# Optimization experiments

Measured on AMD Instinct MI355X. Metric: run time of the kernel, lower is better.

## Reference

```python
import jax, jax.numpy as jnp
import numpy as np
import math

CHUNK = 64

def _linear(x, W, b):
    # torch nn.Linear: y = x @ W.T + b
    return jnp.einsum('bsd,ed->bse', x, W) + b

def setup_inputs() -> dict:
    key = jax.random.key(0)
    ks = jax.random.split(key, 10)
    B, S, D = 4, 4096, 512
    scale = 0.02
    inp = {
        'x': jax.random.normal(ks[0], (B, S, D), jnp.float32),
        'base_phases': jax.random.normal(ks[1], (S, D), jnp.float32) * math.pi,
        'Wk': jax.random.normal(ks[2], (D, D), jnp.float32) * scale,
        'bk': jnp.zeros((D,), jnp.float32),
        'Wv': jax.random.normal(ks[3], (D, D), jnp.float32) * scale,
        'bv': jnp.zeros((D,), jnp.float32),
        'Wq': jax.random.normal(ks[4], (D, D), jnp.float32) * scale,
        'bq': jnp.zeros((D,), jnp.float32),
        'Wkm': jax.random.normal(ks[5], (D, D), jnp.float32) * scale,
        'bkm': jnp.zeros((D,), jnp.float32),
        'Wqm': jax.random.normal(ks[6], (D, D), jnp.float32) * scale,
        'bqm': jnp.zeros((D,), jnp.float32),
        'mod_scale': jnp.ones((1,), jnp.float32) * 0.1,
        'ln_g': jnp.ones((D,), jnp.float32),
        'ln_b': jnp.zeros((D,), jnp.float32),
        'Wo': jax.random.normal(ks[7], (D, D), jnp.float32) * scale,
        'bo': jnp.zeros((D,), jnp.float32),
    }
    return inp

def reference(x, base_phases, Wk, bk, Wv, bv, Wq, bq, Wkm, bkm, Wqm, bqm, mod_scale, ln_g, ln_b, Wo, bo):
    B, S, D = x.shape
    bp = base_phases[:S][None]                      # [1,S,D]
    key = _linear(x, Wk, bk)
    value = _linear(x, Wv, bv)
    query = _linear(x, Wq, bq)
    key_phase = bp + _linear(key, Wkm, bkm) * mod_scale
    query_phase = bp + _linear(query, Wqm, bqm) * mod_scale
    bound_real = value * jnp.cos(key_phase)
    bound_imag = value * jnp.sin(key_phase)
    # chunked cumulative memory (S divisible by CHUNK -> no padding)
    nC = S // CHUNK
    br = bound_real.reshape(B, nC, CHUNK, D)
    bi = bound_imag.reshape(B, nC, CHUNK, D)
    qp = query_phase.reshape(B, nC, CHUNK, D)
    mem_real = jnp.cumsum(br, axis=2)
    mem_imag = jnp.cumsum(bi, axis=2)
    retrieved = (mem_real * jnp.cos(qp) + mem_imag * jnp.sin(qp)).reshape(B, S, D)
    retrieved = retrieved / math.sqrt(D)
    # LayerNorm + Linear (to_out)
    mu = jnp.mean(retrieved, axis=-1, keepdims=True)
    var = jnp.mean((retrieved - mu) ** 2, axis=-1, keepdims=True)
    normed = (retrieved - mu) / jnp.sqrt(var + 1e-5) * ln_g + ln_b
    out = _linear(normed, Wo, bo)
    return x + out
```

## Files before the change

kernel.cpp:

```cpp
#include <hip/hip_runtime.h>
#include <hip/hip_bf16.h>


typedef __attribute__((ext_vector_type(8))) short short8;
typedef __attribute__((ext_vector_type(4))) float f32x4;

#define M_TOK   16384
#define DIM     512
#define NCHUNK  64
#define RPAD    520

__device__ __forceinline__ void gll16(const void* g, void* l) {
  __builtin_amdgcn_global_load_lds(
      (const __attribute__((address_space(1))) unsigned int*)g,
      (__attribute__((address_space(3))) unsigned int*)l, 16, 0, 0);
}

__device__ __forceinline__ uint2 pack4bf(float4 v) {
  union { __hip_bfloat16 h[4]; uint2 u; } t;
  t.h[0] = __float2bfloat16(v.x);
  t.h[1] = __float2bfloat16(v.y);
  t.h[2] = __float2bfloat16(v.z);
  t.h[3] = __float2bfloat16(v.w);
  return t.u;
}

__global__ __launch_bounds__(256) void prep_all(
    const float* __restrict__ x, __hip_bfloat16* __restrict__ x_bf,
    const float* __restrict__ Wv, const float* __restrict__ Wo,
    const float* __restrict__ bv,
    const float* __restrict__ Wkm, const float* __restrict__ Wqm,
    const float* __restrict__ Wk, const float* __restrict__ Wq,
    const float* __restrict__ bk, const float* __restrict__ bkm,
    const float* __restrict__ bq, const float* __restrict__ bqm,
    __hip_bfloat16* __restrict__ Wall, float* __restrict__ bc1,
    __hip_bfloat16* __restrict__ Wm_bf, __hip_bfloat16* __restrict__ WT_bf) {
  const int tid = threadIdx.x;
  if (blockIdx.x < 8192) {
    int i = blockIdx.x * 256 + tid;
    ((uint2*)x_bf)[i] = pack4bf(((const float4*)x)[i]);
    return;
  }
  const int b = blockIdx.x - 8192;
  if (b < 512) {
    int m = b >> 8;
    int idx = ((b & 255) * 256 + tid) * 4;
    const float* src = m ? Wo : Wv;
    __hip_bfloat16* dst = Wall + (m ? (size_t)1536 * 512 : 0);
    ((uint2*)dst)[idx >> 2] = pack4bf(*(const float4*)(src + idx));
    int t = b * 256 + tid;
    if (t < 512) bc1[t] = bv[t];
  } else if (b < 1024) {
    int bb = b - 512;
    int m = bb >> 8;
    int idx = ((bb & 255) * 256 + tid) * 4;
    const float* src = m ? Wqm : Wkm;
    ((uint2*)(Wm_bf + (size_t)m * 262144))[idx >> 2] =
        pack4bf(*(const float4*)(src + idx));
  } else if (b < 1152) {
    __shared__ float tile[64][65];
    int bb = b - 1024;
    int z = bb >> 6;
    int tl = bb & 63;
    int tr = tl >> 3, tc = tl & 7;
    const float* src = z ? Wq : Wk;
#pragma unroll
    for (int i = 0; i < 4; i++) {
      int r = (tid >> 4) + 16 * i;
      int c4 = (tid & 15) * 4;
      float4 v = *(const float4*)(src + (size_t)(tr * 64 + r) * 512 +
                                  tc * 64 + c4);
      tile[r][c4 + 0] = v.x;
      tile[r][c4 + 1] = v.y;
      tile[r][c4 + 2] = v.z;
      tile[r][c4 + 3] = v.w;
    }
    __syncthreads();
    int orow = tid >> 2;
    int seg = tid & 3;
    __hip_bfloat16* dst = WT_bf + (size_t)z * 262144 +
                          (size_t)(tc * 64 + orow) * 512 + tr * 64 + seg * 16;
#pragma unroll
    for (int q = 0; q < 4; q++) {
      float4 v;
      v.x = tile[seg * 16 + q * 4 + 0][orow];
      v.y = tile[seg * 16 + q * 4 + 1][orow];
      v.z = tile[seg * 16 + q * 4 + 2][orow];
      v.w = tile[seg * 16 + q * 4 + 3][orow];
      *(uint2*)(dst + q * 4) = pack4bf(v);
    }
  } else {
    int row = (b - 1152) * 4 + (tid >> 6);
    int lane = tid & 63;
    int z = row >> 9;
    int i = row & 511;
    const float* Wm = z ? Wqm : Wkm;
    const float* b0 = z ? bq : bk;
    const float* bm = z ? bqm : bkm;
    const float4* w4 = (const float4*)(Wm + (size_t)i * 512 + lane * 8);
    const float4* v4 = (const float4*)(b0 + lane * 8);
    float4 w0 = w4[0], w1 = w4[1], c0 = v4[0], c1 = v4[1];
    float acc = w0.x * c0.x + w0.y * c0.y + w0.z * c0.z + w0.w * c0.w +
                w1.x * c1.x + w1.y * c1.y + w1.z * c1.z + w1.w * c1.w;
#pragma unroll
    for (int off = 32; off; off >>= 1) acc += __shfl_xor(acc, off, 64);
    if (lane == 0) bc1[512 + z * 512 + i] = acc + bm[i];
  }
}

__global__ __launch_bounds__(256) void gemm_bt(
    const __hip_bfloat16* __restrict__ A, int lda,
    const __hip_bfloat16* __restrict__ Bt,
    const float* __restrict__ bias,
    __hip_bfloat16* __restrict__ Cout, int ldc) {
  constexpr int K = 512, BK = 32;
  __shared__ __align__(16) __hip_bfloat16 As[128 * BK];
  __shared__ __align__(16) __hip_bfloat16 Bs[128 * BK];

  const int tid  = threadIdx.x;
  const int lane = tid & 63;
  const int w    = tid >> 6;
  const int wm   = w >> 1;
  const int wn   = w & 1;
  const int m0   = blockIdx.y * 128;
  const int n0   = blockIdx.x * 128;

  const int rS0    = (w * 2 + 0) * 16 + (lane >> 2);
  const int rS1    = (w * 2 + 1) * 16 + (lane >> 2);
  const int kInRow = (lane & 3) * 8;
  const __hip_bfloat16* gA0 = A + (size_t)(m0 + rS0) * lda + kInRow;
  const __hip_bfloat16* gA1 = A + (size_t)(m0 + rS1) * lda + kInRow;
  const __hip_bfloat16* gB0 = Bt + (size_t)(n0 + rS0) * K + kInRow;
  const __hip_bfloat16* gB1 = Bt + (size_t)(n0 + rS1) * K + kInRow;
  char* ldsA0 = (char*)As + (w * 2 + 0) * 1024;
  char* ldsA1 = (char*)As + (w * 2 + 1) * 1024;
  char* ldsB0 = (char*)Bs + (w * 2 + 0) * 1024;
  char* ldsB1 = (char*)Bs + (w * 2 + 1) * 1024;

  f32x4 acc[4][4] = {};

  const int rfA = lane & 15;
  const int rfK = (lane >> 4) * 8;

  for (int kt = 0; kt < K; kt += BK) {
    __syncthreads();
    gll16(gA0 + kt, ldsA0);
    gll16(gA1 + kt, ldsA1);
    gll16(gB0 + kt, ldsB0);
    gll16(gB1 + kt, ldsB1);
    __syncthreads();

    short8 af[4], bf[4];
#pragma unroll
    for (int i = 0; i < 4; i++)
      af[i] = *(const short8*)(As + (wm * 64 + i * 16 + rfA) * BK + rfK);
#pragma unroll
    for (int j = 0; j < 4; j++)
      bf[j] = *(const short8*)(Bs + (wn * 64 + j * 16 + rfA) * BK + rfK);
#pragma unroll
    for (int i = 0; i < 4; i++)
#pragma unroll
      for (int j = 0; j < 4; j++)
        acc[i][j] = __builtin_amdgcn_mfma_f32_16x16x32_bf16(
            af[i], bf[j], acc[i][j], 0, 0, 0);
  }

  const int cq = lane >> 4;
#pragma unroll
  for (int i = 0; i < 4; i++) {
    int row = m0 + wm * 64 + i * 16 + cq * 4;
#pragma unroll
    for (int j = 0; j < 4; j++) {
      int col = n0 + wn * 64 + j * 16 + (lane & 15);
      float bz = bias[col];
#pragma unroll
      for (int r = 0; r < 4; r++) {
        float v = acc[i][j][r] + bz;
        Cout[(size_t)(row + r) * ldc + col] = __float2bfloat16(v);
      }
    }
  }
}

__global__ __launch_bounds__(256) void gemm_compose(
    const __hip_bfloat16* __restrict__ Wm_bf,
    const __hip_bfloat16* __restrict__ WT_bf,
    __hip_bfloat16* __restrict__ Wall) {
  constexpr int K = 512, BK = 32;
  const __hip_bfloat16* A  = Wm_bf + (size_t)blockIdx.z * 262144;
  const __hip_bfloat16* Bt = WT_bf + (size_t)blockIdx.z * 262144;
  __hip_bfloat16* C = Wall + (size_t)(512 + blockIdx.z * 512) * 512;
  __shared__ __align__(16) __hip_bfloat16 As[128 * BK];
  __shared__ __align__(16) __hip_bfloat16 Bs[128 * BK];

  const int tid  = threadIdx.x;
  const int lane = tid & 63;
  const int w    = tid >> 6;
  const int wm   = w >> 1;
  const int wn   = w & 1;
  const int m0   = blockIdx.y * 128;
  const int n0   = blockIdx.x * 128;

  const int rS0    = (w * 2 + 0) * 16 + (lane >> 2);
  const int rS1    = (w * 2 + 1) * 16 + (lane >> 2);
  const int kInRow = (lane & 3) * 8;
  const __hip_bfloat16* gA0 = A + (size_t)(m0 + rS0) * K + kInRow;
  const __hip_bfloat16* gA1 = A + (size_t)(m0 + rS1) * K + kInRow;
  const __hip_bfloat16* gB0 = Bt + (size_t)(n0 + rS0) * K + kInRow;
  const __hip_bfloat16* gB1 = Bt + (size_t)(n0 + rS1) * K + kInRow;
  char* ldsA0 = (char*)As + (w * 2 + 0) * 1024;
  char* ldsA1 = (char*)As + (w * 2 + 1) * 1024;
  char* ldsB0 = (char*)Bs + (w * 2 + 0) * 1024;
  char* ldsB1 = (char*)Bs + (w * 2 + 1) * 1024;

  f32x4 acc[4][4] = {};
  const int rfA = lane & 15;
  const int rfK = (lane >> 4) * 8;

  for (int kt = 0; kt < K; kt += BK) {
    __syncthreads();
    gll16(gA0 + kt, ldsA0);
    gll16(gA1 + kt, ldsA1);
    gll16(gB0 + kt, ldsB0);
    gll16(gB1 + kt, ldsB1);
    __syncthreads();

    short8 af[4], bf[4];
#pragma unroll
    for (int i = 0; i < 4; i++)
      af[i] = *(const short8*)(As + (wm * 64 + i * 16 + rfA) * BK + rfK);
#pragma unroll
    for (int j = 0; j < 4; j++)
      bf[j] = *(const short8*)(Bs + (wn * 64 + j * 16 + rfA) * BK + rfK);
#pragma unroll
    for (int i = 0; i < 4; i++)
#pragma unroll
      for (int j = 0; j < 4; j++)
        acc[i][j] = __builtin_amdgcn_mfma_f32_16x16x32_bf16(
            af[i], bf[j], acc[i][j], 0, 0, 0);
  }

  const int cq = lane >> 4;
#pragma unroll
  for (int i = 0; i < 4; i++) {
    int row = m0 + wm * 64 + i * 16 + cq * 4;
#pragma unroll
    for (int j = 0; j < 4; j++) {
      int col = n0 + wn * 64 + j * 16 + (lane & 15);
#pragma unroll
      for (int r = 0; r < 4; r++)
        C[(size_t)(row + r) * 512 + col] = __float2bfloat16(acc[i][j][r]);
    }
  }
}

__global__ __launch_bounds__(1024) void fused_pg(
    const __hip_bfloat16* __restrict__ VKQ,
    const float* __restrict__ bp,
    const float* __restrict__ mod_scale,
    const float* __restrict__ ln_g, const float* __restrict__ ln_b,
    const __hip_bfloat16* __restrict__ WoB,
    const float* __restrict__ bo,
    const float* __restrict__ x,
    float* __restrict__ out) {
  __shared__ __hip_bfloat16 R[64 * RPAD];
  __shared__ float Tr[512], Ti[512];
  const int tid    = threadIdx.x;
  const int seg    = tid >> 9;
  const int d      = tid & 511;
  const int blk    = blockIdx.x;
  const int token0 = blk * 64;
  const int sg0    = (blk & (NCHUNK - 1)) * 64;
  const float msc  = mod_scale[0];
  const float isd  = 0.044194173824159216f;

  {
    const int s0 = seg * 32;
    float mr = 0.f, mi = 0.f;
    const __hip_bfloat16* vb = VKQ + (size_t)(token0 + s0) * 1536 + d;
    const float* bb = bp + (size_t)(sg0 + s0) * 512 + d;
#pragma unroll 4
    for (int s = 0; s < 32; ++s) {
      float v  = __bfloat162float(vb[(size_t)s * 1536]);
      float km = __bfloat162float(vb[(size_t)s * 1536 + 512]);
      float qm = __bfloat162float(vb[(size_t)s * 1536 + 1024]);
      float b  = bb[(size_t)s * 512];
      float kp = b + km * msc;
      float qp = b + qm * msc;
      float sk, ck, sq, cq;
      __sincosf(kp, &sk, &ck);
      __sincosf(qp, &sq, &cq);
      mr += v * ck;
      mi += v * sk;
      R[(s0 + s) * RPAD + d] = __float2bfloat16((mr * cq + mi * sq) * isd);
    }
    if (seg == 0) {
      Tr[d] = mr;
      Ti[d] = mi;
    }
  }
  __syncthreads();

  {
    const int r0 = 32 + seg * 16;
    const float pr = Tr[d] * isd;
    const float pi = Ti[d] * isd;
    const __hip_bfloat16* qb = VKQ + (size_t)(token0 + r0) * 1536 + 1024 + d;
    const float* bb = bp + (size_t)(sg0 + r0) * 512 + d;
#pragma unroll 4
    for (int s = 0; s < 16; ++s) {
      float qm = __bfloat162float(qb[(size_t)s * 1536]);
      float b  = bb[(size_t)s * 512];
      float qp = b + qm * msc;
      float sq, cq;
      __sincosf(qp, &sq, &cq);
      int idx = (r0 + s) * RPAD + d;
      float v = __bfloat162float(R[idx]) + pr * cq + pi * sq;
      R[idx] = __float2bfloat16(v);
    }
  }
  __syncthreads();

  {
    const int lane = tid & 63;
    const int wv   = tid >> 6;
    float gj[8], bj[8];
#pragma unroll
    for (int j = 0; j < 8; j++) {
      int col = lane + 64 * j;
      gj[j] = ln_g[col];
      bj[j] = ln_b[col];
    }
    for (int rr = 0; rr < 4; ++rr) {
      int row = wv * 4 + rr;
      float vals[8], sum = 0.f, sq2 = 0.f;
#pragma unroll
      for (int j = 0; j < 8; j++) {
        float v = __bfloat162float(R[row * RPAD + lane + 64 * j]);
        vals[j] = v;
        sum += v;
        sq2 += v * v;
      }
#pragma unroll
      for (int off = 32; off; off >>= 1) {
        sum += __shfl_xor(sum, off, 64);
        sq2 += __shfl_xor(sq2, off, 64);
      }
      float mu   = sum * (1.f / 512.f);
      float var  = sq2 * (1.f / 512.f) - mu * mu;
      float rstd = rsqrtf(var + 1e-5f);
#pragma unroll
      for (int j = 0; j < 8; j++) {
        float nv = (vals[j] - mu) * rstd * gj[j] + bj[j];
        R[row * RPAD + lane + 64 * j] = __float2bfloat16(nv);
      }
    }
  }
  __syncthreads();

  {
    const int lane = tid & 63;
    const int w    = tid >> 6;
    const int rfA  = lane & 15;
    const int rfK  = (lane >> 4) * 8;
    f32x4 acc[4][2] = {};

    for (int kt = 0; kt < 512; kt += 32) {
      short8 af[4], bf[2];
#pragma unroll
      for (int j = 0; j < 2; j++) {
        int col = w * 32 + j * 16 + rfA;
        bf[j] = *(const short8*)(WoB + (size_t)col * 512 + kt + rfK);
      }
#pragma unroll
      for (int i = 0; i < 4; i++)
        af[i] = *(const short8*)(R + (i * 16 + rfA) * RPAD + kt + rfK);
#pragma unroll
      for (int i = 0; i < 4; i++)
#pragma unroll
        for (int j = 0; j < 2; j++)
          acc[i][j] = __builtin_amdgcn_mfma_f32_16x16x32_bf16(
              af[i], bf[j], acc[i][j], 0, 0, 0);
    }

    const int cq = lane >> 4;
    float bz[2];
#pragma unroll
    for (int j = 0; j < 2; j++) bz[j] = bo[w * 32 + j * 16 + (lane & 15)];
#pragma unroll
    for (int i = 0; i < 4; i++) {
      int row = token0 + i * 16 + cq * 4;
#pragma unroll
      for (int j = 0; j < 2; j++) {
        int col = w * 32 + j * 16 + (lane & 15);
#pragma unroll
        for (int r = 0; r < 4; r++) {
          size_t o = (size_t)(row + r) * 512 + col;
          out[o] = acc[i][j][r] + bz[j] + x[o];
        }
      }
    }
  }
}

extern "C" void kernel_launch(void* const* d_in, const int* in_sizes, int n_in,
                              void* d_out, int out_size, void* d_ws,
                              size_t ws_size, hipStream_t stream) {
  const float* x    = (const float*)d_in[0];
  const float* bp   = (const float*)d_in[1];
  const float* Wk   = (const float*)d_in[2];
  const float* bk   = (const float*)d_in[3];
  const float* Wv   = (const float*)d_in[4];
  const float* bv   = (const float*)d_in[5];
  const float* Wq   = (const float*)d_in[6];
  const float* bq   = (const float*)d_in[7];
  const float* Wkm  = (const float*)d_in[8];
  const float* bkm  = (const float*)d_in[9];
  const float* Wqm  = (const float*)d_in[10];
  const float* bqm  = (const float*)d_in[11];
  const float* msc  = (const float*)d_in[12];
  const float* lng  = (const float*)d_in[13];
  const float* lnb  = (const float*)d_in[14];
  const float* Wo   = (const float*)d_in[15];
  const float* bo   = (const float*)d_in[16];
  float* out = (float*)d_out;

  char* ws = (char*)d_ws;
  __hip_bfloat16* x_bf  = (__hip_bfloat16*)ws;  ws += (size_t)M_TOK * DIM * 2;
  __hip_bfloat16* Wall  = (__hip_bfloat16*)ws;  ws += (size_t)2048 * 512 * 2;
  __hip_bfloat16* Wm_bf = (__hip_bfloat16*)ws;  ws += (size_t)2 * 262144 * 2;
  __hip_bfloat16* WT_bf = (__hip_bfloat16*)ws;  ws += (size_t)2 * 262144 * 2;
  float*          bc1   = (float*)ws;           ws += 1536 * 4;
  __hip_bfloat16* VKQ   = (__hip_bfloat16*)ws;  ws += (size_t)M_TOK * 1536 * 2;

  prep_all<<<9600, 256, 0, stream>>>(x, x_bf, Wv, Wo, bv, Wkm, Wqm, Wk, Wq,
                                     bk, bkm, bq, bqm, Wall, bc1, Wm_bf,
                                     WT_bf);
  gemm_compose<<<dim3(4, 4, 2), 256, 0, stream>>>(Wm_bf, WT_bf, Wall);
  gemm_bt<<<dim3(12, 128), 256, 0, stream>>>(x_bf, DIM, Wall, bc1, VKQ, 1536);
  fused_pg<<<256, 1024, 0, stream>>>(VKQ, bp, msc, lng, lnb,
                                     Wall + (size_t)1536 * 512, bo, x, out);
}
```

Measured before the change: 203.7 us.

## Restructure chunk scan: LDS-staged coalesced loads, 4 segments, cached query trig

The chunked phase-memory scan in the fused kernel changes shape. Each thread now owns two adjacent dims across 4 sequence segments of 16 rows, instead of 2 segments of 32 rows. Rows of V/K/Q and base phases are staged through shared memory with 16-byte coalesced loads, and base phases are converted to bf16 on the way in. The prefix fix-up reuses the query cos/sin kept in registers instead of reloading and recomputing them. This shortens the serial scan and removes uncoalesced strided global loads and repeated sincos, at the cost of more barriers, extra LDS, register pressure, and bf16 rounding of the base phases.

```diff
diff --git a/kernel.cpp b/kernel.cpp
--- a/kernel.cpp
+++ b/kernel.cpp
@@ -7,7 +7,6 @@
 
 #define M_TOK   16384
 #define DIM     512
-#define NCHUNK  64
 #define RPAD    520
 
 __device__ __forceinline__ void gll16(const void* g, void* l) {
@@ -23,6 +22,20 @@
   t.h[2] = __float2bfloat16(v.z);
   t.h[3] = __float2bfloat16(v.w);
   return t.u;
+}
+
+__device__ __forceinline__ unsigned packbf2(float a, float b) {
+  union { __hip_bfloat16 h[2]; unsigned u; } t;
+  t.h[0] = __float2bfloat16(a);
+  t.h[1] = __float2bfloat16(b);
+  return t.u;
+}
+
+__device__ __forceinline__ float bflo(unsigned u) {
+  union { unsigned x; float f; } t; t.x = u << 16; return t.f;
+}
+__device__ __forceinline__ float bfhi(unsigned u) {
+  union { unsigned x; float f; } t; t.x = u & 0xffff0000u; return t.f;
 }
 
 __global__ __launch_bounds__(256) void prep_all(
@@ -63,13 +76,12 @@
     int z = bb >> 6;
     int tl = bb & 63;
     int tr = tl >> 3, tc = tl & 7;
-    const float* src = z ? Wq : Wk;
 #pragma unroll
     for (int i = 0; i < 4; i++) {
       int r = (tid >> 4) + 16 * i;
       int c4 = (tid & 15) * 4;
-      float4 v = *(const float4*)(src + (size_t)(tr * 64 + r) * 512 +
-                                  tc * 64 + c4);
+      float4 v = *(const float4*)((z ? Wq : Wk) +
+                                  (size_t)(tr * 64 + r) * 512 + tc * 64 + c4);
       tile[r][c4 + 0] = v.x;
       tile[r][c4 + 1] = v.y;
       tile[r][c4 + 2] = v.z;
@@ -81,13 +93,13 @@
     __hip_bfloat16* dst = WT_bf + (size_t)z * 262144 +
                           (size_t)(tc * 64 + orow) * 512 + tr * 64 + seg * 16;
 #pragma unroll
-    for (int q = 0; q < 4; q++) {
+    for (int qq = 0; qq < 4; qq++) {
       float4 v;
-      v.x = tile[seg * 16 + q * 4 + 0][orow];
-      v.y = tile[seg * 16 + q * 4 + 1][orow];
-      v.z = tile[seg * 16 + q * 4 + 2][orow];
-      v.w = tile[seg * 16 + q * 4 + 3][orow];
-      *(uint2*)(dst + q * 4) = pack4bf(v);
+      v.x = tile[seg * 16 + qq * 4 + 0][orow];
+      v.y = tile[seg * 16 + qq * 4 + 1][orow];
+      v.z = tile[seg * 16 + qq * 4 + 2][orow];
+      v.w = tile[seg * 16 + qq * 4 + 3][orow];
+      *(uint2*)(dst + qq * 4) = pack4bf(v);
     }
   } else {
     int row = (b - 1152) * 4 + (tid >> 6);
@@ -254,7 +266,7 @@
   }
 }
 
-__global__ __launch_bounds__(1024) void fused_pg(
+__global__ __launch_bounds__(1024) void fused_pg2(
     const __hip_bfloat16* __restrict__ VKQ,
     const float* __restrict__ bp,
     const float* __restrict__ mod_scale,
@@ -263,60 +275,100 @@
     const float* __restrict__ bo,
     const float* __restrict__ x,
     float* __restrict__ out) {
-  __shared__ __hip_bfloat16 R[64 * RPAD];
-  __shared__ float Tr[512], Ti[512];
+  __shared__ __align__(16) __hip_bfloat16 SP[4][16][RPAD];
+  __shared__ __align__(16) __hip_bfloat16 R[64 * RPAD];
+  __shared__ float Tpre[3][2][512];
   const int tid    = threadIdx.x;
-  const int seg    = tid >> 9;
-  const int d      = tid & 511;
-  const int blk    = blockIdx.x;
-  const int token0 = blk * 64;
-  const int sg0    = (blk & (NCHUNK - 1)) * 64;
+  const int token0 = blockIdx.x * 64;
+  const int sg0    = (blockIdx.x & 63) * 64;
   const float msc  = mod_scale[0];
   const float isd  = 0.044194173824159216f;
 
-  {
-    const int s0 = seg * 32;
-    float mr = 0.f, mi = 0.f;
-    const __hip_bfloat16* vb = VKQ + (size_t)(token0 + s0) * 1536 + d;
-    const float* bb = bp + (size_t)(sg0 + s0) * 512 + d;
-#pragma unroll 4
-    for (int s = 0; s < 32; ++s) {
-      float v  = __bfloat162float(vb[(size_t)s * 1536]);
-      float km = __bfloat162float(vb[(size_t)s * 1536 + 512]);
-      float qm = __bfloat162float(vb[(size_t)s * 1536 + 1024]);
-      float b  = bb[(size_t)s * 512];
-      float kp = b + km * msc;
-      float qp = b + qm * msc;
-      float sk, ck, sq, cq;
-      __sincosf(kp, &sk, &ck);
-      __sincosf(qp, &sq, &cq);
-      mr += v * ck;
-      mi += v * sk;
-      R[(s0 + s) * RPAD + d] = __float2bfloat16((mr * cq + mi * sq) * isd);
-    }
-    if (seg == 0) {
-      Tr[d] = mr;
-      Ti[d] = mi;
-    }
+  const int seg = tid >> 8;
+  const int d0  = (tid & 255) * 2;
+
+  const int ssl  = tid >> 6;
+  const int sm   = tid & 63;
+  const int sseg = ssl >> 2;
+  const int sj   = ssl & 3;
+
+  float mr0 = 0.f, mi0 = 0.f, mr1 = 0.f, mi1 = 0.f;
+  unsigned qt0[16], qt1[16];
+
+#pragma unroll
+  for (int w = 0; w < 4; ++w) {
+    __syncthreads();
+    {
+      int srow = sseg * 16 + w * 4 + sj;
+      const __hip_bfloat16* g =
+          VKQ + (size_t)(token0 + srow) * 1536 + sm * 8;
+      *(uint4*)&SP[0][ssl][sm * 8] = *(const uint4*)(g);
+      *(uint4*)&SP[1][ssl][sm * 8] = *(const uint4*)(g + 512);
+      *(uint4*)&SP[2][ssl][sm * 8] = *(const uint4*)(g + 1024);
+      const float* gb = bp + (size_t)(sg0 + srow) * 512 + sm * 8;
+      float4 b0 = *(const float4*)gb;
+      float4 b1 = *(const float4*)(gb + 4);
+      uint4 pb;
+      pb.x = packbf2(b0.x, b0.y);
+      pb.y = packbf2(b0.z, b0.w);
+      pb.z = packbf2(b1.x, b1.y);
+      pb.w = packbf2(b1.z, b1.w);
+      *(uint4*)&SP[3][ssl][sm * 8] = pb;
+    }
+    __syncthreads();
+#pragma unroll
+    for (int j = 0; j < 4; ++j) {
+      int sl = seg * 4 + j;
+      unsigned uv = *(const unsigned*)&SP[0][sl][d0];
+      unsigned uk = *(const unsigned*)&SP[1][sl][d0];
+      unsigned uq = *(const unsigned*)&SP[2][sl][d0];
+      unsigned ub = *(const unsigned*)&SP[3][sl][d0];
+      float v0 = bflo(uv), v1 = bfhi(uv);
+      float k0 = bflo(uk), k1 = bfhi(uk);
+      float q0 = bflo(uq), q1 = bfhi(uq);
+      float b0 = bflo(ub), b1 = bfhi(ub);
+      float kp0 = b0 + k0 * msc, qp0 = b0 + q0 * msc;
+      float kp1 = b1 + k1 * msc, qp1 = b1 + q1 * msc;
+      float sk0, ck0, sq0, cq0, sk1, ck1, sq1, cq1;
+      __sincosf(kp0, &sk0, &ck0);
+      __sincosf(qp0, &sq0, &cq0);
+      __sincosf(kp1, &sk1, &ck1);
+      __sincosf(qp1, &sq1, &cq1);
+      mr0 += v0 * ck0; mi0 += v0 * sk0;
+      mr1 += v1 * ck1; mi1 += v1 * sk1;
+      float r0 = (mr0 * cq0 + mi0 * sq0) * isd;
+      float r1 = (mr1 * cq1 + mi1 * sq1) * isd;
+      int s = seg * 16 + w * 4 + j;
+      *(unsigned*)&R[s * RPAD + d0] = packbf2(r0, r1);
+      int si = w * 4 + j;
+      if (seg > 0) {
+        qt0[si] = packbf2(cq0, sq0);
+        qt1[si] = packbf2(cq1, sq1);
+      }
+    }
+  }
+  if (seg < 3) {
+    Tpre[seg][0][d0]     = mr0 * isd;
+    Tpre[seg][0][d0 + 1] = mr1 * isd;
+    Tpre[seg][1][d0]     = mi0 * isd;
+    Tpre[seg][1][d0 + 1] = mi1 * isd;
   }
   __syncthreads();
-
-  {
-    const int r0 = 32 + seg * 16;
-    const float pr = Tr[d] * isd;
-    const float pi = Ti[d] * isd;
-    const __hip_bfloat16* qb = VKQ + (size_t)(token0 + r0) * 1536 + 1024 + d;
-    const float* bb = bp + (size_t)(sg0 + r0) * 512 + d;
-#pragma unroll 4
-    for (int s = 0; s < 16; ++s) {
-      float qm = __bfloat162float(qb[(size_t)s * 1536]);
-      float b  = bb[(size_t)s * 512];
-      float qp = b + qm * msc;
-      float sq, cq;
-      __sincosf(qp, &sq, &cq);
-      int idx = (r0 + s) * RPAD + d;
-      float v = __bfloat162float(R[idx]) + pr * cq + pi * sq;
-      R[idx] = __float2bfloat16(v);
+  if (seg > 0) {
+    float Pr0 = 0.f, Pi0 = 0.f, Pr1 = 0.f, Pi1 = 0.f;
+    for (int k = 0; k < seg; ++k) {
+      Pr0 += Tpre[k][0][d0];
+      Pr1 += Tpre[k][0][d0 + 1];
+      Pi0 += Tpre[k][1][d0];
+      Pi1 += Tpre[k][1][d0 + 1];
+    }
+#pragma unroll
+    for (int si = 0; si < 16; ++si) {
+      int s = seg * 16 + si;
+      unsigned ur = *(const unsigned*)&R[s * RPAD + d0];
+      float r0 = bflo(ur) + Pr0 * bflo(qt0[si]) + Pi0 * bfhi(qt0[si]);
+      float r1 = bfhi(ur) + Pr1 * bflo(qt1[si]) + Pi1 * bfhi(qt1[si]);
+      *(unsigned*)&R[s * RPAD + d0] = packbf2(r0, r1);
     }
   }
   __syncthreads();
@@ -360,16 +412,17 @@
 
   {
     const int lane = tid & 63;
-    const int w    = tid >> 6;
+    const int wv   = tid >> 6;
     const int rfA  = lane & 15;
     const int rfK  = (lane >> 4) * 8;
+    const int dw0  = wv * 32;
     f32x4 acc[4][2] = {};
 
     for (int kt = 0; kt < 512; kt += 32) {
       short8 af[4], bf[2];
 #pragma unroll
       for (int j = 0; j < 2; j++) {
-        int col = w * 32 + j * 16 + rfA;
+        int col = dw0 + j * 16 + rfA;
         bf[j] = *(const short8*)(WoB + (size_t)col * 512 + kt + rfK);
       }
 #pragma unroll
@@ -386,13 +439,13 @@
     const int cq = lane >> 4;
     float bz[2];
 #pragma unroll
-    for (int j = 0; j < 2; j++) bz[j] = bo[w * 32 + j * 16 + (lane & 15)];
+    for (int j = 0; j < 2; j++) bz[j] = bo[dw0 + j * 16 + (lane & 15)];
 #pragma unroll
     for (int i = 0; i < 4; i++) {
       int row = token0 + i * 16 + cq * 4;
 #pragma unroll
       for (int j = 0; j < 2; j++) {
-        int col = w * 32 + j * 16 + (lane & 15);
+        int col = dw0 + j * 16 + (lane & 15);
 #pragma unroll
         for (int r = 0; r < 4; r++) {
           size_t o = (size_t)(row + r) * 512 + col;
@@ -438,6 +491,6 @@
                                      WT_bf);
   gemm_compose<<<dim3(4, 4, 2), 256, 0, stream>>>(Wm_bf, WT_bf, Wall);
   gemm_bt<<<dim3(12, 128), 256, 0, stream>>>(x_bf, DIM, Wall, bc1, VKQ, 1536);
-  fused_pg<<<256, 1024, 0, stream>>>(VKQ, bp, msc, lng, lnb,
-                                     Wall + (size_t)1536 * 512, bo, x, out);
-}
+  fused_pg2<<<256, 1024, 0, stream>>>(VKQ, bp, msc, lng, lnb,
+                                      Wall + (size_t)1536 * 512, bo, x, out);
+}
```

Result: slower. 212.3 us (+4.3%).
